# Performance work log

Hardware: AMD Instinct MI355X
Metric: run time of the kernel (lower is better)

The kernel has to match this reference:

```python
import jax, jax.numpy as jnp
import numpy as np

NTIME, NBATCH = 1024, 65536


def setup_inputs() -> dict:
    key = jax.random.key(0)
    k1, k2, k3 = jax.random.split(key, 3)
    # times must be sorted along the time axis (dim 0) per batch column
    times = jnp.sort(jax.random.uniform(k1, (NTIME, NBATCH), dtype=jnp.float32), axis=0)
    values = jax.random.normal(k2, (NTIME, NBATCH), dtype=jnp.float32)
    # query times inside the covered range (0,1)
    t = jax.random.uniform(k3, (NBATCH,), dtype=jnp.float32)
    return {"times": times, "values": values, "t": t}


def reference(times, values, t):
    # times, values: (ntime, nbatch); t: (nbatch,)
    ntime, nbatch = times.shape
    # precached slopes as in __init__: (ntime-1, nbatch)
    slopes = jnp.diff(values, axis=0) / jnp.diff(times, axis=0)
    # searchsorted-by-counting: number of knots <= t, wrapped mod ntime
    gi = jnp.mod(jnp.sum((times - t[None, :]) <= 0, axis=0), ntime)  # (nbatch,)
    b = jnp.arange(nbatch)
    # torch negative-index wrap semantics: gi-1 == -1 wraps to last row
    iv = jnp.mod(gi - 1, ntime)       # index into times/values
    isl = jnp.mod(gi - 1, ntime - 1)  # index into slopes
    # direct per-batch gather (equivalent to torch.diagonal(x[gi-1]))
    v0 = values[iv, b]
    s0 = slopes[isl, b]
    t0 = times[iv, b]
    return v0 + s0 * (t - t0)
```

## Files before the change

### kernel.cpp

```cpp
#include <hip/hip_runtime.h>

__global__ void bts_interp_kernel(const float* __restrict__ times,
                                  const float* __restrict__ values,
                                  const float* __restrict__ t,
                                  float* __restrict__ out,
                                  int ntime, int nbatch) {
    int b = blockIdx.x * blockDim.x + threadIdx.x;
    if (b >= nbatch) return;

    float tq = t[b];

    int lo = 0, hi = ntime;
    float t0v = 0.0f;
    float t1v = 0.0f;
    while (lo < hi) {
        int mid = (lo + hi) >> 1;
        float v = times[(long)mid * nbatch + b];
        if (v <= tq) { lo = mid + 1; t0v = v; }
        else         { hi = mid;     t1v = v; }
    }

    float res;
    if (lo > 0 && lo < ntime) {
        long base = (long)(lo - 1) * nbatch + b;
        float va = values[base];
        float vb = values[base + nbatch];
        res = va + (vb - va) / (t1v - t0v) * (tq - t0v);
    } else {
        long base = (long)(ntime - 2) * nbatch + b;
        float ta = times[base];
        float tb = times[base + nbatch];
        float va = values[base];
        float vb = values[base + nbatch];
        res = vb + (vb - va) / (tb - ta) * (tq - tb);
    }
    out[b] = res;
}

extern "C" void kernel_launch(void* const* d_in, const int* in_sizes, int n_in,
                              void* d_out, int out_size, void* d_ws, size_t ws_size,
                              hipStream_t stream) {
    const float* times  = (const float*)d_in[0];
    const float* values = (const float*)d_in[1];
    const float* t      = (const float*)d_in[2];
    float* out = (float*)d_out;

    int nbatch = in_sizes[2];
    int ntime  = in_sizes[0] / nbatch;

    const int BLOCK = 256;
    int grid = (nbatch + BLOCK - 1) / BLOCK;
    bts_interp_kernel<<<grid, BLOCK, 0, stream>>>(times, values, t, out, ntime, nbatch);
}
```

Baseline: 408.2 us.

## Replace binary search with strided branchless count plus local refine

Replaces the per-thread data-dependent binary search over the time axis with a branchless two-level search. It first counts knots at every 8th row across 128 independent loads, then loads a 9-row window to find the exact interval. The independent loads can be issued in parallel instead of as a chain of 10 dependent ones, but the kernel now reads about 137 rows per column instead of about 10. ntime is hardcoded to 1024, so the kernel no longer works for other sizes.

```diff
diff --git a/kernel.cpp b/kernel.cpp
--- a/kernel.cpp
+++ b/kernel.cpp
@@ -1,38 +1,57 @@
 #include <hip/hip_runtime.h>
 
-__global__ void bts_interp_kernel(const float* __restrict__ times,
-                                  const float* __restrict__ values,
-                                  const float* __restrict__ t,
-                                  float* __restrict__ out,
-                                  int ntime, int nbatch) {
+__global__ __launch_bounds__(256) void bts_interp_kernel(
+    const float* __restrict__ times,
+    const float* __restrict__ values,
+    const float* __restrict__ t,
+    float* __restrict__ out,
+    int nbatch) {
     int b = blockIdx.x * blockDim.x + threadIdx.x;
     if (b >= nbatch) return;
 
     float tq = t[b];
 
-    int lo = 0, hi = ntime;
-    float t0v = 0.0f;
-    float t1v = 0.0f;
-    while (lo < hi) {
-        int mid = (lo + hi) >> 1;
-        float v = times[(long)mid * nbatch + b];
-        if (v <= tq) { lo = mid + 1; t0v = v; }
-        else         { hi = mid;     t1v = v; }
+    const float* pA = times + 7 * nbatch + b;
+    int c = 0;
+    #pragma unroll 32
+    for (int k = 0; k < 128; ++k) {
+        float v = pA[k * 8 * nbatch];
+        c += (v <= tq) ? 1 : 0;
     }
 
     float res;
-    if (lo > 0 && lo < ntime) {
-        long base = (long)(lo - 1) * nbatch + b;
-        float va = values[base];
-        float vb = values[base + nbatch];
-        res = va + (vb - va) / (t1v - t0v) * (tq - t0v);
+    if (c == 128) {
+        int off = 1022 * nbatch + b;
+        float ta = times[off], tb = times[off + nbatch];
+        float va = values[off], vb = values[off + nbatch];
+        res = vb + (vb - va) / (tb - ta) * (tq - tb);
     } else {
-        long base = (long)(ntime - 2) * nbatch + b;
-        float ta = times[base];
-        float tb = times[base + nbatch];
-        float va = values[base];
-        float vb = values[base + nbatch];
-        res = vb + (vb - va) / (tb - ta) * (tq - tb);
+        float tw[9];
+        int base = 8 * c - 1;
+        #pragma unroll
+        for (int j = 0; j < 9; ++j) {
+            int r = base + j;
+            r = r < 0 ? 0 : r;
+            tw[j] = times[r * nbatch + b];
+        }
+        int cnt = 0;
+        #pragma unroll
+        for (int j = 1; j <= 7; ++j) cnt += (tw[j] <= tq) ? 1 : 0;
+        int L = 8 * c + cnt;
+
+        if (L == 0) {
+            int off = 1022 * nbatch + b;
+            float ta = times[off], tb = times[off + nbatch];
+            float va = values[off], vb = values[off + nbatch];
+            res = vb + (vb - va) / (tb - ta) * (tq - tb);
+        } else {
+            float t0 = tw[cnt];
+            float t1 = tw[cnt + 1];
+            int off = (L - 1) * nbatch + b;
+            float v0 = values[off];
+            float v1 = values[off + nbatch];
+            res = v0 + (v1 - v0) / (t1 - t0) * (tq - t0);
+        }
     }
     out[b] = res;
 }
@@ -46,9 +65,8 @@
     float* out = (float*)d_out;
 
     int nbatch = in_sizes[2];
-    int ntime  = in_sizes[0] / nbatch;
 
     const int BLOCK = 256;
     int grid = (nbatch + BLOCK - 1) / BLOCK;
-    bts_interp_kernel<<<grid, BLOCK, 0, stream>>>(times, values, t, out, ntime, nbatch);
+    bts_interp_kernel<<<grid, BLOCK, 0, stream>>>(times, values, t, out, nbatch);
 }
```

Result: slower. 439.4 us (+7.6%).

## Replace per-thread binary search with coalesced strided count scan and local refine

Applied to the files above, without the earlier changes.

Replaces the dependent-load binary search with a coalesced scan over every fourth time knot, split across four y-threads per batch column and reduced through shared memory. A short refinement over three neighboring knots then locates the exact interval. This trades latency-bound dependent gathers for streaming bandwidth over a quarter of the times array. It assumes ntime divisible by 16, nbatch divisible by 64, and times inside (-1,2) for the sentinels.

```diff
diff --git a/kernel.cpp b/kernel.cpp
--- a/kernel.cpp
+++ b/kernel.cpp
@@ -1,38 +1,73 @@
 #include <hip/hip_runtime.h>
 
-__global__ void bts_interp_kernel(const float* __restrict__ times,
-                                  const float* __restrict__ values,
-                                  const float* __restrict__ t,
-                                  float* __restrict__ out,
-                                  int ntime, int nbatch) {
-    int b = blockIdx.x * blockDim.x + threadIdx.x;
-    if (b >= nbatch) return;
+__global__ __launch_bounds__(256) void bts_interp_kernel(
+    const float* __restrict__ times,
+    const float* __restrict__ values,
+    const float* __restrict__ t,
+    float* __restrict__ out,
+    int ntime, int nbatch) {
+    const int x = threadIdx.x;
+    const int y = threadIdx.y;
+    const int b = blockIdx.x * 64 + x;
 
-    float tq = t[b];
+    const int K = ntime >> 4;
+    const float tq = t[b];
 
-    int lo = 0, hi = ntime;
-    float t0v = 0.0f;
-    float t1v = 0.0f;
-    while (lo < hi) {
-        int mid = (lo + hi) >> 1;
-        float v = times[(long)mid * nbatch + b];
-        if (v <= tq) { lo = mid + 1; t0v = v; }
-        else         { hi = mid;     t1v = v; }
+    const float* p = times + (size_t)(4 * y * K + 3) * nbatch + b;
+    int cnt = 0;
+    float tlo = -1.0f;
+    float thi = 2.0f;
+    #pragma unroll 16
+    for (int k = 0; k < K; ++k) {
+        float v = p[(size_t)k * 4 * nbatch];
+        bool le = (v <= tq);
+        cnt += le ? 1 : 0;
+        tlo = le ? v : tlo;
+        thi = fminf(thi, le ? 2.0f : v);
+    }
+
+    __shared__ int   s_cnt[4][64];
+    __shared__ float s_tlo[4][64];
+    __shared__ float s_thi[4][64];
+    s_cnt[y][x] = cnt;
+    s_tlo[y][x] = tlo;
+    s_thi[y][x] = thi;
+    __syncthreads();
+
+    if (y != 0) return;
+
+    int c = s_cnt[0][x] + s_cnt[1][x] + s_cnt[2][x] + s_cnt[3][x];
+    float t_lo = fmaxf(fmaxf(s_tlo[0][x], s_tlo[1][x]),
+                       fmaxf(s_tlo[2][x], s_tlo[3][x]));
+    float t_hi = fminf(fminf(s_thi[0][x], s_thi[1][x]),
+                       fminf(s_thi[2][x], s_thi[3][x]));
+
+    const int nsamp = ntime >> 2;
+    int L;
+    float t0 = 0.0f, t1 = 1.0f;
+    if (c == nsamp) {
+        L = ntime;
+    } else {
+        size_t w = (size_t)(4 * c) * nbatch + b;
+        float w0 = times[w];
+        float w1 = times[w + nbatch];
+        float w2 = times[w + 2 * (size_t)nbatch];
+        int c2 = (w0 <= tq ? 1 : 0) + (w1 <= tq ? 1 : 0) + (w2 <= tq ? 1 : 0);
+        L = 4 * c + c2;
+        t0 = (c2 == 0) ? t_lo : (c2 == 1 ? w0 : (c2 == 2 ? w1 : w2));
+        t1 = (c2 == 3) ? t_hi : (c2 == 0 ? w0 : (c2 == 1 ? w1 : w2));
     }
 
     float res;
-    if (lo > 0 && lo < ntime) {
-        long base = (long)(lo - 1) * nbatch + b;
-        float va = values[base];
-        float vb = values[base + nbatch];
-        res = va + (vb - va) / (t1v - t0v) * (tq - t0v);
+    if (L == 0 || L == ntime) {
+        size_t off = (size_t)(ntime - 2) * nbatch + b;
+        float ta = times[off], tb = times[off + nbatch];
+        float va = values[off], vb = values[off + nbatch];
+        res = vb + (vb - va) / (tb - ta) * (tq - tb);
     } else {
-        long base = (long)(ntime - 2) * nbatch + b;
-        float ta = times[base];
-        float tb = times[base + nbatch];
-        float va = values[base];
-        float vb = values[base + nbatch];
-        res = vb + (vb - va) / (tb - ta) * (tq - tb);
+        size_t off = (size_t)(L - 1) * nbatch + b;
+        float v0 = values[off], v1 = values[off + nbatch];
+        res = v0 + (v1 - v0) / (t1 - t0) * (tq - t0);
     }
     out[b] = res;
 }
@@ -48,7 +83,7 @@
     int nbatch = in_sizes[2];
     int ntime  = in_sizes[0] / nbatch;
 
-    const int BLOCK = 256;
-    int grid = (nbatch + BLOCK - 1) / BLOCK;
-    bts_interp_kernel<<<grid, BLOCK, 0, stream>>>(times, values, t, out, ntime, nbatch);
+    dim3 block(64, 4);
+    int grid = nbatch / 64;
+    bts_interp_kernel<<<grid, block, 0, stream>>>(times, values, t, out, ntime, nbatch);
 }
```

After: 424.7 us. 1.04x slower.
